# Kernel optimization log

Measured on AMD Instinct MI355X. Metric: run time of the kernel, lower is better.

## Reference

```python
import jax, jax.numpy as jnp
import numpy as np

RADIUS = 0.2
NSAMPLE = 32
GROUPS = 4
EPS = 1e-5


def group_norm(x, gamma, beta):
    # x: [B, C, *spatial]; normalize per (batch, group) over channels-in-group + spatial
    B, C = x.shape[0], x.shape[1]
    rest = x.shape[2:]
    xr = x.reshape(B, GROUPS, -1)
    mean = xr.mean(-1, keepdims=True)
    var = xr.var(-1, keepdims=True)
    xr = (xr - mean) * jax.lax.rsqrt(var + EPS)
    x = xr.reshape((B, C) + rest)
    bshape = (1, C) + (1,) * len(rest)
    return x * gamma.reshape(bshape) + beta.reshape(bshape)


def ball_query(pos_t):
    # pos_t: [B, N, 3] -> idx [B, N, NSAMPLE] (query points == all points)
    N = pos_t.shape[1]
    sq = jnp.sum(pos_t * pos_t, axis=-1)  # [B, N]
    d = sq[:, :, None] + sq[:, None, :] - 2.0 * jnp.einsum('bnc,bmc->bnm', pos_t, pos_t)
    ar = jnp.arange(N, dtype=jnp.int32)
    gi = jnp.where(d > RADIUS * RADIUS, N, ar[None, None, :])  # [B, S, N]
    gi = jnp.sort(gi, axis=-1)[:, :, :NSAMPLE]  # ascending in-ball indices first
    first = gi[:, :, :1]
    gi = jnp.where(gi == N, first, gi)  # pad with first neighbor
    return gi


def setup_inputs() -> dict:
    key = jax.random.key(0)
    ks = jax.random.split(key, 6)
    B, C, N = 2, 64, 4096
    M = 4 * C  # mid channels
    return {
        'x': jax.random.normal(ks[0], (B, C, N), jnp.float32),
        'pos': jax.random.uniform(ks[1], (B, 3, N), jnp.float32),
        'w1': jax.random.normal(ks[2], (M, C), jnp.float32) * 0.05,
        'b1': jnp.zeros((M,), jnp.float32),
        'g1': jnp.ones((M,), jnp.float32),
        'be1': jnp.zeros((M,), jnp.float32),
        'wd': 1.0 + jax.random.normal(ks[3], (M,), jnp.float32) * 0.05,
        'gd': jnp.ones((M,), jnp.float32),
        'bed': jnp.zeros((M,), jnp.float32),
        'w2': jax.random.normal(ks[4], (C, M), jnp.float32) * 0.05,
        'b2': jnp.zeros((C,), jnp.float32),
        'g2': jnp.ones((C,), jnp.float32),
        'be2': jnp.zeros((C,), jnp.float32),
    }


def reference(x, pos, w1, b1, g1, be1, wd, gd, bed, w2, b2, g2, be2):
    # x: [B, C, N], pos: [B, 3, N]
    pos_t = jnp.transpose(pos, (0, 2, 1))  # [B, N, 3]
    idx = ball_query(pos_t)  # [B, N, K]

    # conv1 (1x1) -> GroupNorm -> GELU
    h = jnp.einsum('mc,bcn->bmn', w1, x) + b1[None, :, None]
    h = jax.nn.gelu(group_norm(h, g1, be1), approximate=False)  # [B, M, N]

    # gather neighbors: feats [B, N, M] indexed by idx [B, N, K]
    feats = jnp.transpose(h, (0, 2, 1))
    grouped = jax.vmap(lambda f, i: f[i])(feats, idx)  # [B, N, K, M]
    grouped = jnp.transpose(grouped, (0, 3, 1, 2))  # [B, M, N, K]

    # depthwise 1x1 conv (per-channel scale, no bias) -> GroupNorm -> max-pool over K -> GELU
    grouped = grouped * wd[None, :, None, None]
    grouped = group_norm(grouped, gd, bed)
    h2 = jax.nn.gelu(jnp.max(grouped, axis=-1), approximate=False)  # [B, M, N]

    # conv2 (1x1) -> GroupNorm -> residual
    out = jnp.einsum('cm,bmn->bcn', w2, h2) + b2[None, :, None]
    out = group_norm(out, g2, be2)
    return out + x
```

## Files before the change

kernel.cpp:

```cpp
#include <hip/hip_runtime.h>
#include <hip/hip_fp16.h>
#include <math.h>

#define BB 2
#define CC 64
#define NN 4096
#define MM 256
#define KK 32
#define GG 4
#define EPSF 1e-5f

__device__ __forceinline__ float gelu_exact(float x) {
    return 0.5f * x * (1.0f + erff(x * 0.70710678118654752f));
}

__device__ __forceinline__ unsigned pkmax(unsigned a, unsigned b) {
    unsigned d;
    asm("v_pk_max_f16 %0, %1, %2" : "=v"(d) : "v"(a), "v"(b));
    return d;
}
__device__ __forceinline__ unsigned pkmin(unsigned a, unsigned b) {
    unsigned d;
    asm("v_pk_min_f16 %0, %1, %2" : "=v"(d) : "v"(a), "v"(b));
    return d;
}
__device__ __forceinline__ unsigned selpair(unsigned mx, unsigned mn, float g0, float g1) {
    unsigned lo = (g0 >= 0.f) ? (mx & 0x0000FFFFu) : (mn & 0x0000FFFFu);
    unsigned hi = (g1 >= 0.f) ? (mx & 0xFFFF0000u) : (mn & 0xFFFF0000u);
    return lo | hi;
}
__device__ __forceinline__ float bcast_lane(float v, int lane) {
    return __int_as_float(__builtin_amdgcn_readlane(__float_as_int(v), lane));
}

__global__ void k_mlp1(const float* __restrict__ x, const float* __restrict__ w1,
                       const float* __restrict__ b1, __half* __restrict__ hH,
                       float2* __restrict__ Mp) {
    __shared__ float xs[64 * 128];
    __shared__ float w1t[64 * 32];
    __shared__ float r1[4], r2[4];

    int bx = blockIdx.x;
    int nt = bx & 31, mt = (bx >> 5) & 7, b = bx >> 8;
    int n0 = nt * 128, m0 = mt * 32;
    int t = threadIdx.x;

    {
        int nq = t & 31, ch = t >> 5;
        #pragma unroll
        for (int p = 0; p < 8; p++) {
            int c = p * 8 + ch;
            float4 v = *(const float4*)&x[((size_t)(b * CC + c)) * NN + n0 + nq * 4];
            *(float4*)&xs[c * 128 + nq * 4] = v;
        }
    }
    {
        #pragma unroll
        for (int p = 0; p < 2; p++) {
            int idx = p * 256 + t;
            int m = idx >> 4, cq = idx & 15;
            float4 v = *(const float4*)&w1[(m0 + m) * CC + cq * 4];
            w1t[(cq * 4 + 0) * 32 + m] = v.x;
            w1t[(cq * 4 + 1) * 32 + m] = v.y;
            w1t[(cq * 4 + 2) * 32 + m] = v.z;
            w1t[(cq * 4 + 3) * 32 + m] = v.w;
        }
    }
    __syncthreads();

    int nq = t & 31;
    int mseg = t >> 5;
    float o[4][4];
    #pragma unroll
    for (int i = 0; i < 4; i++)
        #pragma unroll
        for (int j = 0; j < 4; j++) o[i][j] = 0.f;

    for (int c = 0; c < 64; c++) {
        float4 xv = *(float4*)&xs[c * 128 + nq * 4];
        float4 wv = *(float4*)&w1t[c * 32 + mseg * 4];
        o[0][0] = fmaf(wv.x, xv.x, o[0][0]); o[0][1] = fmaf(wv.x, xv.y, o[0][1]);
        o[0][2] = fmaf(wv.x, xv.z, o[0][2]); o[0][3] = fmaf(wv.x, xv.w, o[0][3]);
        o[1][0] = fmaf(wv.y, xv.x, o[1][0]); o[1][1] = fmaf(wv.y, xv.y, o[1][1]);
        o[1][2] = fmaf(wv.y, xv.z, o[1][2]); o[1][3] = fmaf(wv.y, xv.w, o[1][3]);
        o[2][0] = fmaf(wv.z, xv.x, o[2][0]); o[2][1] = fmaf(wv.z, xv.y, o[2][1]);
        o[2][2] = fmaf(wv.z, xv.z, o[2][2]); o[2][3] = fmaf(wv.z, xv.w, o[2][3]);
        o[3][0] = fmaf(wv.w, xv.x, o[3][0]); o[3][1] = fmaf(wv.w, xv.y, o[3][1]);
        o[3][2] = fmaf(wv.w, xv.z, o[3][2]); o[3][3] = fmaf(wv.w, xv.w, o[3][3]);
    }

    float s1 = 0.f, s2 = 0.f;
    #pragma unroll
    for (int mi = 0; mi < 4; mi++) {
        int m = m0 + mseg * 4 + mi;
        float bv = b1[m];
        float4 r;
        r.x = o[mi][0] + bv; r.y = o[mi][1] + bv;
        r.z = o[mi][2] + bv; r.w = o[mi][3] + bv;
        __half2 hA = __float22half2_rn(make_float2(r.x, r.y));
        __half2 hB = __float22half2_rn(make_float2(r.z, r.w));
        uint2 st8;
        st8.x = *(unsigned*)&hA; st8.y = *(unsigned*)&hB;
        *(uint2*)((char*)hH + (((size_t)(b * MM + m)) * NN + n0 + nq * 4) * 2) = st8;
        s1 += r.x + r.y + r.z + r.w;
        s2 = fmaf(r.x, r.x, s2); s2 = fmaf(r.y, r.y, s2);
        s2 = fmaf(r.z, r.z, s2); s2 = fmaf(r.w, r.w, s2);
    }
    for (int off = 32; off; off >>= 1) {
        s1 += __shfl_down(s1, off, 64);
        s2 += __shfl_down(s2, off, 64);
    }
    int w = t >> 6, l = t & 63;
    if (l == 0) { r1[w] = s1; r2[w] = s2; }
    __syncthreads();
    if (t == 0) {
        Mp[bx] = make_float2(r1[0] + r1[1] + r1[2] + r1[3],
                             r2[0] + r2[1] + r2[2] + r2[3]);
    }
}

__global__ void k_gn1t_ballq(const __half* __restrict__ hH, const float* __restrict__ g1,
                             const float* __restrict__ be1, const float* __restrict__ wd,
                             const float2* __restrict__ Mp, __half* __restrict__ pH,
                             float* __restrict__ R,
                             const float* __restrict__ pos, int* __restrict__ idx) {
    __shared__ float tile[64 * 65];
    __shared__ float mv[2];
    int t = threadIdx.x;

    if (blockIdx.x < 512) {
        int id = blockIdx.x;
        int n0 = (id & 63) * 64;
        int g  = (id >> 6) & 3;
        int b  = id >> 8;
        int m0 = g * 64;

        if (t < 64) {
            float2 p2 = Mp[b * 256 + g * 64 + t];
            float s1 = p2.x, s2 = p2.y;
            for (int off = 32; off; off >>= 1) {
                s1 += __shfl_down(s1, off, 64);
                s2 += __shfl_down(s2, off, 64);
            }
            if (t == 0) {
                const double cnt = 64.0 * 4096.0;
                double md = (double)s1 / cnt;
                double vd = (double)s2 / cnt - md * md;
                mv[0] = (float)md;
                mv[1] = rsqrtf((float)vd + EPSF);
            }
        }
        __syncthreads();
        float mean = mv[0], rstd = mv[1];

        int nq = t & 15, mr = t >> 4;
        #pragma unroll
        for (int pp = 0; pp < 4; pp++) {
            int row = pp * 16 + mr;
            int m = m0 + row;
            float a = rstd * g1[m];
            float cc2 = be1[m] - mean * a;
            float wdm = wd[m];
            uint2 raw = *(const uint2*)((const char*)hH +
                         (((size_t)(b * MM + m)) * NN + n0 + nq * 4) * 2);
            float2 fa = __half22float2(*(__half2*)&raw.x);
            float2 fb = __half22float2(*(__half2*)&raw.y);
            tile[row * 65 + nq * 4 + 0] = gelu_exact(fmaf(fa.x, a, cc2)) * wdm;
            tile[row * 65 + nq * 4 + 1] = gelu_exact(fmaf(fa.y, a, cc2)) * wdm;
            tile[row * 65 + nq * 4 + 2] = gelu_exact(fmaf(fb.x, a, cc2)) * wdm;
            tile[row * 65 + nq * 4 + 3] = gelu_exact(fmaf(fb.y, a, cc2)) * wdm;
        }
        __syncthreads();
        #pragma unroll
        for (int pp = 0; pp < 4; pp++) {
            int id2 = pp * 256 + t;
            int nl = id2 >> 4, mq = id2 & 15;
            float a0 = tile[(mq * 4 + 0) * 65 + nl];
            float a1 = tile[(mq * 4 + 1) * 65 + nl];
            float a2 = tile[(mq * 4 + 2) * 65 + nl];
            float a3 = tile[(mq * 4 + 3) * 65 + nl];
            __half2 hA = __float22half2_rn(make_float2(a0, a1));
            __half2 hB = __float22half2_rn(make_float2(a2, a3));
            uint2 st8;
            st8.x = *(unsigned*)&hA; st8.y = *(unsigned*)&hB;
            *(uint2*)((char*)pH + ((((size_t)(b * NN) + n0 + nl)) << 9) + (m0 + mq * 4) * 2) = st8;
            float2 fa = __half22float2(hA);
            float2 fb = __half22float2(hB);
            float t1 = fa.x + fa.y + fb.x + fb.y;
            float t2 = fa.x * fa.x + fa.y * fa.y + fb.x * fb.x + fb.y * fb.y;
            #pragma unroll
            for (int off = 8; off; off >>= 1) {
                t1 += __shfl_down(t1, off, 16);
                t2 += __shfl_down(t2, off, 16);
            }
            if ((t & 15) == 0) {
                float* rr = &R[((size_t)(b * NN) + n0 + nl) * 8];
                rr[g]     = t1;
                rr[4 + g] = t2;
            }
        }
    } else {
        int bx = blockIdx.x - 512;
        int wid  = bx * 4 + (threadIdx.x >> 6);
        int lane = threadIdx.x & 63;
        int b = wid >> 12;
        int n = wid & 4095;
        const float* px = pos + b * 3 * NN;
        const float* py = px + NN;
        const float* pz = py + NN;
        float qx = px[n], qy = py[n], qz = pz[n];
        float qsq = qx*qx + qy*qy + qz*qz;
        int* row = idx + (b * NN + n) * KK;

        int found = 0;
        int first = -1;
        const float R2 = 0.04f;
        for (int m0 = 0; m0 < NN && found < KK; m0 += 64) {
            int m = m0 + lane;
            float ax = px[m], ay = py[m], az = pz[m];
            float msq = ax*ax + ay*ay + az*az;
            float dot = qx*ax + qy*ay + qz*az;
            float d = qsq + msq - 2.0f * dot;
            bool hit = !(d > R2);
            unsigned long long mask = __ballot(hit);
            if (first < 0 && mask) first = m0 + (__ffsll((long long)mask) - 1);
            unsigned long long lt = (lane == 0) ? 0ULL : (mask & ((1ULL << lane) - 1ULL));
            int posh = __popcll(lt);
            if (hit && (found + posh) < KK) row[found + posh] = m;
            found += __popcll(mask);
            if (found > KK) found = KK;
        }
        if (lane < KK && lane >= found) row[lane] = first;
    }
}

__global__ void k_gstats(const int* __restrict__ idx, const float* __restrict__ R,
                         float* __restrict__ Gp) {
    __shared__ float sAcc[8][8];
    int t = threadIdx.x;
    int bid = blockIdx.x;
    int hw = t >> 5, cl = t & 31;
    int pbase = bid * 32;
    int b = pbase >> 12;
    float s[8];
    #pragma unroll
    for (int c = 0; c < 8; c++) s[c] = 0.f;
    #pragma unroll
    for (int it = 0; it < 4; it++) {
        int pt = pbase + it * 8 + hw;
        int j = idx[pt * KK + cl];
        const float* rr = &R[((size_t)(b * NN) + j) * 8];
        float4 ra = *(const float4*)rr;
        float4 rb = *(const float4*)(rr + 4);
        s[0] += ra.x; s[1] += ra.y; s[2] += ra.z; s[3] += ra.w;
        s[4] += rb.x; s[5] += rb.y; s[6] += rb.z; s[7] += rb.w;
    }
    #pragma unroll
    for (int off = 16; off; off >>= 1) {
        #pragma unroll
        for (int c = 0; c < 8; c++) s[c] += __shfl_down(s[c], off, 32);
    }
    if (cl == 0) {
        #pragma unroll
        for (int c = 0; c < 8; c++) sAcc[hw][c] = s[c];
    }
    __syncthreads();
    if (t < 8) {
        float v = 0.f;
        #pragma unroll
        for (int k = 0; k < 8; k++) v += sAcc[k][t];
        Gp[bid * 8 + t] = v;
    }
}

__global__ __launch_bounds__(256, 2)
void k_mlp2g(const __half* __restrict__ pH, const int* __restrict__ idx,
             const float* __restrict__ Gp, const float* __restrict__ w2,
             const float* __restrict__ b2, const float* __restrict__ gd,
             const float* __restrict__ bed, float* __restrict__ oraw,
             float* __restrict__ Op) {
    __shared__ float w2s[64 * 257];
    __shared__ uint4 phs4[4][4][32];
    __shared__ float sw[4][8];
    __shared__ float sA[4][4], sB[4][4];

    int t = threadIdx.x;
    int w = t >> 6, l = t & 63;
    int q = blockIdx.x;
    int b = ((q & 7) < 4) ? 0 : 1;
    int local = (q >> 3) * 4 + (q & 3);
    int n0 = local * 16 + w * 4;

    #pragma unroll
    for (int p = 0; p < 16; p++) {
        int i = p * 256 + t;
        int c = i >> 6, mq = i & 63;
        float4 v = ((const float4*)w2)[i];
        float* dst = &w2s[c * 257 + mq * 4];
        dst[0] = v.x; dst[1] = v.y; dst[2] = v.z; dst[3] = v.w;
    }

    {
        float s[8] = {0.f, 0.f, 0.f, 0.f, 0.f, 0.f, 0.f, 0.f};
        if (t < 128) {
            const float4* gp = (const float4*)(Gp + ((size_t)(b * 128 + t)) * 8);
            float4 ra = gp[0], rb = gp[1];
            s[0] = ra.x; s[1] = ra.y; s[2] = ra.z; s[3] = ra.w;
            s[4] = rb.x; s[5] = rb.y; s[6] = rb.z; s[7] = rb.w;
        }
        #pragma unroll
        for (int off = 32; off; off >>= 1) {
            #pragma unroll
            for (int c = 0; c < 8; c++) s[c] += __shfl_down(s[c], off, 64);
        }
        if (l == 0) {
            #pragma unroll
            for (int c = 0; c < 8; c++) sw[w][c] = s[c];
        }
    }
    __syncthreads();

    int g = l >> 4;
    double s1 = (double)sw[0][g] + sw[1][g] + sw[2][g] + sw[3][g];
    double s2 = (double)sw[0][4 + g] + sw[1][4 + g] + sw[2][4 + g] + sw[3][4 + g];
    const double cnt2 = 64.0 * 4096.0 * 32.0;
    double m_ = s1 / cnt2;
    double v_ = s2 / cnt2 - m_ * m_;
    float mean = (float)m_;
    float rstd = rsqrtf((float)v_ + EPSF);
    float4 gd4  = ((const float4*)gd)[l];
    float4 bed4 = ((const float4*)bed)[l];
    float ax = rstd * gd4.x, ay = rstd * gd4.y, az = rstd * gd4.z, aw = rstd * gd4.w;
    float cx = bed4.x - mean * ax, cy = bed4.y - mean * ay;
    float cz = bed4.z - mean * az, cw = bed4.w - mean * aw;

    {
        int hh = l >> 5, cl = l & 31;
        const char* pb = (const char*)(pH + (size_t)b * NN * 256);
        int laneoff = cl * 16;
        const float4* g4 = (const float4*)gd;
        float4 gA = g4[cl * 2], gB = g4[cl * 2 + 1];
        #pragma unroll
        for (int p = 0; p < 4; p++) {
            int myidx = idx[((size_t)(b * NN) + n0 + p) * KK + cl];
            unsigned vmax0 = 0xFC00FC00u, vmax1 = 0xFC00FC00u, vmax2 = 0xFC00FC00u, vmax3 = 0xFC00FC00u;
            unsigned vmin0 = 0x7C007C00u, vmin1 = 0x7C007C00u, vmin2 = 0x7C007C00u, vmin3 = 0x7C007C00u;
            #pragma unroll
            for (int kb = 0; kb < 4; kb++) {
                int jj[4];
                #pragma unroll
                for (int u = 0; u < 4; u++) {
                    int k = kb * 4 + u;
                    int ja = __shfl(myidx, 2 * k, 64);
                    int jb = __shfl(myidx, 2 * k + 1, 64);
                    jj[u] = hh ? jb : ja;
                }
                uint4 r[4];
                #pragma unroll
                for (int u = 0; u < 4; u++)
                    r[u] = *(const uint4*)(pb + (((size_t)jj[u]) << 9) + laneoff);
                #pragma unroll
                for (int u = 0; u < 4; u++) {
                    vmax0 = pkmax(vmax0, r[u].x); vmin0 = pkmin(vmin0, r[u].x);
                    vmax1 = pkmax(vmax1, r[u].y); vmin1 = pkmin(vmin1, r[u].y);
                    vmax2 = pkmax(vmax2, r[u].z); vmin2 = pkmin(vmin2, r[u].z);
                    vmax3 = pkmax(vmax3, r[u].w); vmin3 = pkmin(vmin3, r[u].w);
                }
            }
            vmax0 = pkmax(vmax0, (unsigned)__shfl_xor((int)vmax0, 32, 64));
            vmax1 = pkmax(vmax1, (unsigned)__shfl_xor((int)vmax1, 32, 64));
            vmax2 = pkmax(vmax2, (unsigned)__shfl_xor((int)vmax2, 32, 64));
            vmax3 = pkmax(vmax3, (unsigned)__shfl_xor((int)vmax3, 32, 64));
            vmin0 = pkmin(vmin0, (unsigned)__shfl_xor((int)vmin0, 32, 64));
            vmin1 = pkmin(vmin1, (unsigned)__shfl_xor((int)vmin1, 32, 64));
            vmin2 = pkmin(vmin2, (unsigned)__shfl_xor((int)vmin2, 32, 64));
            vmin3 = pkmin(vmin3, (unsigned)__shfl_xor((int)vmin3, 32, 64));

            if (hh == 0) {
                uint4 o4;
                o4.x = selpair(vmax0, vmin0, gA.x, gA.y);
                o4.y = selpair(vmax1, vmin1, gA.z, gA.w);
                o4.z = selpair(vmax2, vmin2, gB.x, gB.y);
                o4.w = selpair(vmax3, vmin3, gB.z, gB.w);
                phs4[w][p][cl] = o4;
            }
        }
    }

    float4 h2r[4];
    #pragma unroll
    for (int j = 0; j < 4; j++) {
        const uint2* pr = (const uint2*)&phs4[w][j][0];
        uint2 raw = pr[l];
        float2 fa = __half22float2(*(__half2*)&raw.x);
        float2 fb = __half22float2(*(__half2*)&raw.y);
        h2r[j].x = gelu_exact(fmaf(fa.x, ax, cx));
        h2r[j].y = gelu_exact(fmaf(fa.y, ay, cy));
        h2r[j].z = gelu_exact(fmaf(fb.x, az, cz));
        h2r[j].w = gelu_exact(fmaf(fb.y, aw, cw));
    }

    const float* w2l = &w2s[l * 257];
    float acc[4] = {0.f, 0.f, 0.f, 0.f};
    #pragma unroll 8
    for (int mq = 0; mq < 64; mq++) {
        float w0  = w2l[4 * mq + 0];
        float w1_ = w2l[4 * mq + 1];
        float w2_ = w2l[4 * mq + 2];
        float w3_ = w2l[4 * mq + 3];
        #pragma unroll
        for (int j = 0; j < 4; j++) {
            acc[j] = fmaf(w0,  bcast_lane(h2r[j].x, mq), acc[j]);
            acc[j] = fmaf(w1_, bcast_lane(h2r[j].y, mq), acc[j]);
            acc[j] = fmaf(w2_, bcast_lane(h2r[j].z, mq), acc[j]);
            acc[j] = fmaf(w3_, bcast_lane(h2r[j].w, mq), acc[j]);
        }
    }

    float bias = b2[l];
    float so1 = 0.f, so2 = 0.f;
    #pragma unroll
    for (int j = 0; j < 4; j++) {
        acc[j] += bias;
        so1 += acc[j];
        so2 = fmaf(acc[j], acc[j], so2);
    }
    *(float4*)&oraw[((size_t)(b * CC) + l) * NN + n0] =
        make_float4(acc[0], acc[1], acc[2], acc[3]);

    so1 += __shfl_down(so1, 8, 16); so2 += __shfl_down(so2, 8, 16);
    so1 += __shfl_down(so1, 4, 16); so2 += __shfl_down(so2, 4, 16);
    so1 += __shfl_down(so1, 2, 16); so2 += __shfl_down(so2, 2, 16);
    so1 += __shfl_down(so1, 1, 16); so2 += __shfl_down(so2, 1, 16);
    if ((l & 15) == 0) { sA[w][l >> 4] = so1; sB[w][l >> 4] = so2; }
    __syncthreads();
    if (t < 8) {
        int is2 = t >> 2, gg = t & 3;
        float v = is2 ? (sB[0][gg] + sB[1][gg] + sB[2][gg] + sB[3][gg])
                      : (sA[0][gg] + sA[1][gg] + sA[2][gg] + sA[3][gg]);
        Op[(b * 256 + local) * 8 + t] = v;
    }
}

__global__ void k_final(const float* __restrict__ oraw, const float* __restrict__ x,
                        const float* __restrict__ g2, const float* __restrict__ be2,
                        const float* __restrict__ Op, float* __restrict__ out) {
    __shared__ float fw[4][8];
    int t = threadIdx.x;
    int i4 = blockIdx.x * 256 + t;
    int base = i4 * 4;
    int b = base >> 18;

    {
        const float4* rp = (const float4*)(Op + ((size_t)(b * 256 + t)) * 8);
        float4 ra = rp[0], rb = rp[1];
        float s[8] = {ra.x, ra.y, ra.z, ra.w, rb.x, rb.y, rb.z, rb.w};
        #pragma unroll
        for (int off = 32; off; off >>= 1) {
            #pragma unroll
            for (int c = 0; c < 8; c++) s[c] += __shfl_down(s[c], off, 64);
        }
        if ((t & 63) == 0) {
            #pragma unroll
            for (int c = 0; c < 8; c++) fw[t >> 6][c] = s[c];
        }
    }
    __syncthreads();

    int c = (base >> 12) & 63;
    int g = c >> 4;
    double s1 = (double)fw[0][g] + fw[1][g] + fw[2][g] + fw[3][g];
    double s2 = (double)fw[0][4 + g] + fw[1][4 + g] + fw[2][4 + g] + fw[3][4 + g];
    const double cnt = 16.0 * 4096.0;
    double mean_d = s1 / cnt;
    double var_d  = s2 / cnt - mean_d * mean_d;
    float mean = (float)mean_d;
    float rstd = rsqrtf((float)var_d + EPSF);
    float sc = rstd * g2[c];
    float ad = be2[c] - mean * sc;
    float4 o = ((const float4*)oraw)[i4];
    float4 xv = ((const float4*)x)[i4];
    float4 r;
    r.x = fmaf(o.x, sc, ad) + xv.x;
    r.y = fmaf(o.y, sc, ad) + xv.y;
    r.z = fmaf(o.z, sc, ad) + xv.z;
    r.w = fmaf(o.w, sc, ad) + xv.w;
    ((float4*)out)[i4] = r;
}

extern "C" void kernel_launch(void* const* d_in, const int* in_sizes, int n_in,
                              void* d_out, int out_size, void* d_ws, size_t ws_size,
                              hipStream_t stream) {
    const float* x   = (const float*)d_in[0];
    const float* pos = (const float*)d_in[1];
    const float* w1  = (const float*)d_in[2];
    const float* b1  = (const float*)d_in[3];
    const float* g1  = (const float*)d_in[4];
    const float* be1 = (const float*)d_in[5];
    const float* wd  = (const float*)d_in[6];
    const float* gd  = (const float*)d_in[7];
    const float* bed = (const float*)d_in[8];
    const float* w2  = (const float*)d_in[9];
    const float* b2  = (const float*)d_in[10];
    const float* g2  = (const float*)d_in[11];
    const float* be2 = (const float*)d_in[12];
    float* out = (float*)d_out;

    char* wsb = (char*)d_ws;
    __half* hH    = (__half*)wsb;
    __half* pH    = (__half*)(wsb + 8388608);
    float*  oraw  = (float*)(wsb + 16777216);
    int*    idx   = (int*)(wsb + 18874368);
    float*  R     = (float*)(wsb + 19922944);
    float2* Mp    = (float2*)(wsb + 20185088);
    float*  Gp    = (float*)(wsb + 20189184);
    float*  Op    = (float*)(wsb + 20197376);

    k_mlp1<<<512, 256, 0, stream>>>(x, w1, b1, hH, Mp);
    k_gn1t_ballq<<<2560, 256, 0, stream>>>(hH, g1, be1, wd, Mp, pH, R, pos, idx);
    k_gstats<<<256, 256, 0, stream>>>(idx, R, Gp);
    k_mlp2g<<<512, 256, 0, stream>>>(pH, idx, Gp, w2, b2, gd, bed, oraw, Op);
    k_final<<<512, 256, 0, stream>>>(oraw, x, g2, be2, Op, out);
}
```

Measured before the change: 146.1 us.

## Fuse ball query into conv1 kernel and compute grouped stats via neighbor counts

Ball query now runs in the same launch as the conv1 GEMM, and each neighbor hit atomically bumps a per-point occurrence count. The GN1/transpose kernel then weights each point's channel-group sums by that count to get the grouped GroupNorm statistics directly. This removes the separate gather-based stats kernel and the per-point R buffer. Conv2 and final stats are now accumulated with global atomics into a small buffer instead of partial arrays reduced again downstream. The cost is many global atomics, a memset launch, and float atomic ordering making the statistics slightly nondeterministic.

Result: slower. 214.5 us (+46.8%).

```diff
diff --git a/kernel.cpp b/kernel.cpp
--- a/kernel.cpp
+++ b/kernel.cpp
@@ -33,171 +33,94 @@
     return __int_as_float(__builtin_amdgcn_readlane(__float_as_int(v), lane));
 }
 
-__global__ void k_mlp1(const float* __restrict__ x, const float* __restrict__ w1,
-                       const float* __restrict__ b1, __half* __restrict__ hH,
-                       float2* __restrict__ Mp) {
-    __shared__ float xs[64 * 128];
-    __shared__ float w1t[64 * 32];
-    __shared__ float r1[4], r2[4];
-
-    int bx = blockIdx.x;
-    int nt = bx & 31, mt = (bx >> 5) & 7, b = bx >> 8;
-    int n0 = nt * 128, m0 = mt * 32;
+__global__ void k_mlp1_ballq(const float* __restrict__ x, const float* __restrict__ w1,
+                             const float* __restrict__ b1, __half* __restrict__ hH,
+                             float2* __restrict__ Mp,
+                             const float* __restrict__ pos, int* __restrict__ idxb,
+                             int* __restrict__ cnt) {
+    __shared__ __align__(16) float xs[64 * 128];
+    __shared__ __align__(16) float w1t[64 * 32];
     int t = threadIdx.x;
 
-    {
-        int nq = t & 31, ch = t >> 5;
+    if (blockIdx.x < 512) {
+        int bx = blockIdx.x;
+        int nt = bx & 31, mt = (bx >> 5) & 7, b = bx >> 8;
+        int n0 = nt * 128, m0 = mt * 32;
+
+        {
+            int nq = t & 31, ch = t >> 5;
+            #pragma unroll
+            for (int p = 0; p < 8; p++) {
+                int c = p * 8 + ch;
+                float4 v = *(const float4*)&x[((size_t)(b * CC + c)) * NN + n0 + nq * 4];
+                *(float4*)&xs[c * 128 + nq * 4] = v;
+            }
+        }
+        {
+            #pragma unroll
+            for (int p = 0; p < 2; p++) {
+                int idx = p * 256 + t;
+                int m = idx >> 4, cq = idx & 15;
+                float4 v = *(const float4*)&w1[(m0 + m) * CC + cq * 4];
+                w1t[(cq * 4 + 0) * 32 + m] = v.x;
+                w1t[(cq * 4 + 1) * 32 + m] = v.y;
+                w1t[(cq * 4 + 2) * 32 + m] = v.z;
+                w1t[(cq * 4 + 3) * 32 + m] = v.w;
+            }
+        }
+        __syncthreads();
+
+        int nq = t & 31;
+        int mseg = t >> 5;
+        float o[4][4];
         #pragma unroll
-        for (int p = 0; p < 8; p++) {
-            int c = p * 8 + ch;
-            float4 v = *(const float4*)&x[((size_t)(b * CC + c)) * NN + n0 + nq * 4];
-            *(float4*)&xs[c * 128 + nq * 4] = v;
-        }
-    }
-    {
+        for (int i = 0; i < 4; i++)
+            #pragma unroll
+            for (int j = 0; j < 4; j++) o[i][j] = 0.f;
+
+        for (int c = 0; c < 64; c++) {
+            float4 xv = *(float4*)&xs[c * 128 + nq * 4];
+            float4 wv = *(float4*)&w1t[c * 32 + mseg * 4];
+            o[0][0] = fmaf(wv.x, xv.x, o[0][0]); o[0][1] = fmaf(wv.x, xv.y, o[0][1]);
+            o[0][2] = fmaf(wv.x, xv.z, o[0][2]); o[0][3] = fmaf(wv.x, xv.w, o[0][3]);
+            o[1][0] = fmaf(wv.y, xv.x, o[1][0]); o[1][1] = fmaf(wv.y, xv.y, o[1][1]);
+            o[1][2] = fmaf(wv.y, xv.z, o[1][2]); o[1][3] = fmaf(wv.y, xv.w, o[1][3]);
+            o[2][0] = fmaf(wv.z, xv.x, o[2][0]); o[2][1] = fmaf(wv.z, xv.y, o[2][1]);
+            o[2][2] = fmaf(wv.z, xv.z, o[2][2]); o[2][3] = fmaf(wv.z, xv.w, o[2][3]);
+            o[3][0] = fmaf(wv.w, xv.x, o[3][0]); o[3][1] = fmaf(wv.w, xv.y, o[3][1]);
+            o[3][2] = fmaf(wv.w, xv.z, o[3][2]); o[3][3] = fmaf(wv.w, xv.w, o[3][3]);
+        }
+
+        float s1 = 0.f, s2 = 0.f;
         #pragma unroll
-        for (int p = 0; p < 2; p++) {
-            int idx = p * 256 + t;
-            int m = idx >> 4, cq = idx & 15;
-            float4 v = *(const float4*)&w1[(m0 + m) * CC + cq * 4];
-            w1t[(cq * 4 + 0) * 32 + m] = v.x;
-            w1t[(cq * 4 + 1) * 32 + m] = v.y;
-            w1t[(cq * 4 + 2) * 32 + m] = v.z;
-            w1t[(cq * 4 + 3) * 32 + m] = v.w;
-        }
-    }
-    __syncthreads();
-
-    int nq = t & 31;
-    int mseg = t >> 5;
-    float o[4][4];
-    #pragma unroll
-    for (int i = 0; i < 4; i++)
-        #pragma unroll
-        for (int j = 0; j < 4; j++) o[i][j] = 0.f;
-
-    for (int c = 0; c < 64; c++) {
-        float4 xv = *(float4*)&xs[c * 128 + nq * 4];
-        float4 wv = *(float4*)&w1t[c * 32 + mseg * 4];
-        o[0][0] = fmaf(wv.x, xv.x, o[0][0]); o[0][1] = fmaf(wv.x, xv.y, o[0][1]);
-        o[0][2] = fmaf(wv.x, xv.z, o[0][2]); o[0][3] = fmaf(wv.x, xv.w, o[0][3]);
-        o[1][0] = fmaf(wv.y, xv.x, o[1][0]); o[1][1] = fmaf(wv.y, xv.y, o[1][1]);
-        o[1][2] = fmaf(wv.y, xv.z, o[1][2]); o[1][3] = fmaf(wv.y, xv.w, o[1][3]);
-        o[2][0] = fmaf(wv.z, xv.x, o[2][0]); o[2][1] = fmaf(wv.z, xv.y, o[2][1]);
-        o[2][2] = fmaf(wv.z, xv.z, o[2][2]); o[2][3] = fmaf(wv.z, xv.w, o[2][3]);
-        o[3][0] = fmaf(wv.w, xv.x, o[3][0]); o[3][1] = fmaf(wv.w, xv.y, o[3][1]);
-        o[3][2] = fmaf(wv.w, xv.z, o[3][2]); o[3][3] = fmaf(wv.w, xv.w, o[3][3]);
-    }
-
-    float s1 = 0.f, s2 = 0.f;
-    #pragma unroll
-    for (int mi = 0; mi < 4; mi++) {
-        int m = m0 + mseg * 4 + mi;
-        float bv = b1[m];
-        float4 r;
-        r.x = o[mi][0] + bv; r.y = o[mi][1] + bv;
-        r.z = o[mi][2] + bv; r.w = o[mi][3] + bv;
-        __half2 hA = __float22half2_rn(make_float2(r.x, r.y));
-        __half2 hB = __float22half2_rn(make_float2(r.z, r.w));
-        uint2 st8;
-        st8.x = *(unsigned*)&hA; st8.y = *(unsigned*)&hB;
-        *(uint2*)((char*)hH + (((size_t)(b * MM + m)) * NN + n0 + nq * 4) * 2) = st8;
-        s1 += r.x + r.y + r.z + r.w;
-        s2 = fmaf(r.x, r.x, s2); s2 = fmaf(r.y, r.y, s2);
-        s2 = fmaf(r.z, r.z, s2); s2 = fmaf(r.w, r.w, s2);
-    }
-    for (int off = 32; off; off >>= 1) {
-        s1 += __shfl_down(s1, off, 64);
-        s2 += __shfl_down(s2, off, 64);
-    }
-    int w = t >> 6, l = t & 63;
-    if (l == 0) { r1[w] = s1; r2[w] = s2; }
-    __syncthreads();
-    if (t == 0) {
-        Mp[bx] = make_float2(r1[0] + r1[1] + r1[2] + r1[3],
-                             r2[0] + r2[1] + r2[2] + r2[3]);
-    }
-}
-
-__global__ void k_gn1t_ballq(const __half* __restrict__ hH, const float* __restrict__ g1,
-                             const float* __restrict__ be1, const float* __restrict__ wd,
-                             const float2* __restrict__ Mp, __half* __restrict__ pH,
-                             float* __restrict__ R,
-                             const float* __restrict__ pos, int* __restrict__ idx) {
-    __shared__ float tile[64 * 65];
-    __shared__ float mv[2];
-    int t = threadIdx.x;
-
-    if (blockIdx.x < 512) {
-        int id = blockIdx.x;
-        int n0 = (id & 63) * 64;
-        int g  = (id >> 6) & 3;
-        int b  = id >> 8;
-        int m0 = g * 64;
-
-        if (t < 64) {
-            float2 p2 = Mp[b * 256 + g * 64 + t];
-            float s1 = p2.x, s2 = p2.y;
-            for (int off = 32; off; off >>= 1) {
-                s1 += __shfl_down(s1, off, 64);
-                s2 += __shfl_down(s2, off, 64);
-            }
-            if (t == 0) {
-                const double cnt = 64.0 * 4096.0;
-                double md = (double)s1 / cnt;
-                double vd = (double)s2 / cnt - md * md;
-                mv[0] = (float)md;
-                mv[1] = rsqrtf((float)vd + EPSF);
-            }
-        }
-        __syncthreads();
-        float mean = mv[0], rstd = mv[1];
-
-        int nq = t & 15, mr = t >> 4;
-        #pragma unroll
-        for (int pp = 0; pp < 4; pp++) {
-            int row = pp * 16 + mr;
-            int m = m0 + row;
-            float a = rstd * g1[m];
-            float cc2 = be1[m] - mean * a;
-            float wdm = wd[m];
-            uint2 raw = *(const uint2*)((const char*)hH +
-                         (((size_t)(b * MM + m)) * NN + n0 + nq * 4) * 2);
-            float2 fa = __half22float2(*(__half2*)&raw.x);
-            float2 fb = __half22float2(*(__half2*)&raw.y);
-            tile[row * 65 + nq * 4 + 0] = gelu_exact(fmaf(fa.x, a, cc2)) * wdm;
-            tile[row * 65 + nq * 4 + 1] = gelu_exact(fmaf(fa.y, a, cc2)) * wdm;
-            tile[row * 65 + nq * 4 + 2] = gelu_exact(fmaf(fb.x, a, cc2)) * wdm;
-            tile[row * 65 + nq * 4 + 3] = gelu_exact(fmaf(fb.y, a, cc2)) * wdm;
-        }
-        __syncthreads();
-        #pragma unroll
-        for (int pp = 0; pp < 4; pp++) {
-            int id2 = pp * 256 + t;
-            int nl = id2 >> 4, mq = id2 & 15;
-            float a0 = tile[(mq * 4 + 0) * 65 + nl];
-            float a1 = tile[(mq * 4 + 1) * 65 + nl];
-            float a2 = tile[(mq * 4 + 2) * 65 + nl];
-            float a3 = tile[(mq * 4 + 3) * 65 + nl];
-            __half2 hA = __float22half2_rn(make_float2(a0, a1));
-            __half2 hB = __float22half2_rn(make_float2(a2, a3));
+        for (int mi = 0; mi < 4; mi++) {
+            int m = m0 + mseg * 4 + mi;
+            float bv = b1[m];
+            float4 r;
+            r.x = o[mi][0] + bv; r.y = o[mi][1] + bv;
+            r.z = o[mi][2] + bv; r.w = o[mi][3] + bv;
+            __half2 hA = __float22half2_rn(make_float2(r.x, r.y));
+            __half2 hB = __float22half2_rn(make_float2(r.z, r.w));
             uint2 st8;
             st8.x = *(unsigned*)&hA; st8.y = *(unsigned*)&hB;
-            *(uint2*)((char*)pH + ((((size_t)(b * NN) + n0 + nl)) << 9) + (m0 + mq * 4) * 2) = st8;
-            float2 fa = __half22float2(hA);
-            float2 fb = __half22float2(hB);
-            float t1 = fa.x + fa.y + fb.x + fb.y;
-            float t2 = fa.x * fa.x + fa.y * fa.y + fb.x * fb.x + fb.y * fb.y;
-            #pragma unroll
-            for (int off = 8; off; off >>= 1) {
-                t1 += __shfl_down(t1, off, 16);
-                t2 += __shfl_down(t2, off, 16);
-            }
-            if ((t & 15) == 0) {
-                float* rr = &R[((size_t)(b * NN) + n0 + nl) * 8];
-                rr[g]     = t1;
-                rr[4 + g] = t2;
-            }
+            *(uint2*)((char*)hH + (((size_t)(b * MM + m)) * NN + n0 + nq * 4) * 2) = st8;
+            s1 += r.x + r.y + r.z + r.w;
+            s2 = fmaf(r.x, r.x, s2); s2 = fmaf(r.y, r.y, s2);
+            s2 = fmaf(r.z, r.z, s2); s2 = fmaf(r.w, r.w, s2);
+        }
+        for (int off = 32; off; off >>= 1) {
+            s1 += __shfl_down(s1, off, 64);
+            s2 += __shfl_down(s2, off, 64);
+        }
+        __syncthreads();
+        float* r1 = w1t;
+        float* r2 = w1t + 4;
+        int w = t >> 6, l = t & 63;
+        if (l == 0) { r1[w] = s1; r2[w] = s2; }
+        __syncthreads();
+        if (t == 0) {
+            Mp[bx] = make_float2(r1[0] + r1[1] + r1[2] + r1[3],
+                                 r2[0] + r2[1] + r2[2] + r2[3]);
         }
     } else {
         int bx = blockIdx.x - 512;
@@ -210,7 +133,8 @@
         const float* pz = py + NN;
         float qx = px[n], qy = py[n], qz = pz[n];
         float qsq = qx*qx + qy*qy + qz*qz;
-        int* row = idx + (b * NN + n) * KK;
+        int* row = idxb + (b * NN + n) * KK;
+        int* cb = cnt + b * NN;
 
         int found = 0;
         int first = -1;
@@ -226,62 +150,113 @@
             if (first < 0 && mask) first = m0 + (__ffsll((long long)mask) - 1);
             unsigned long long lt = (lane == 0) ? 0ULL : (mask & ((1ULL << lane) - 1ULL));
             int posh = __popcll(lt);
-            if (hit && (found + posh) < KK) row[found + posh] = m;
+            if (hit && (found + posh) < KK) {
+                row[found + posh] = m;
+                atomicAdd(&cb[m], 1);
+            }
             found += __popcll(mask);
             if (found > KK) found = KK;
         }
         if (lane < KK && lane >= found) row[lane] = first;
-    }
-}
-
-__global__ void k_gstats(const int* __restrict__ idx, const float* __restrict__ R,
-                         float* __restrict__ Gp) {
-    __shared__ float sAcc[8][8];
+        if (lane == 0 && found < KK) atomicAdd(&cb[first], KK - found);
+    }
+}
+
+__global__ void k_gn1t(const __half* __restrict__ hH, const float* __restrict__ g1,
+                       const float* __restrict__ be1, const float* __restrict__ wd,
+                       const float2* __restrict__ Mp, __half* __restrict__ pH,
+                       const int* __restrict__ cnt, float* __restrict__ GpS) {
+    __shared__ float tile[64 * 65];
+    __shared__ float mv[2];
+    __shared__ float sAcc1, sAcc2;
     int t = threadIdx.x;
-    int bid = blockIdx.x;
-    int hw = t >> 5, cl = t & 31;
-    int pbase = bid * 32;
-    int b = pbase >> 12;
-    float s[8];
+
+    int id = blockIdx.x;
+    int n0 = (id & 63) * 64;
+    int g  = (id >> 6) & 3;
+    int b  = id >> 8;
+    int m0 = g * 64;
+
+    if (t == 0) { sAcc1 = 0.f; sAcc2 = 0.f; }
+    if (t < 64) {
+        float2 p2 = Mp[b * 256 + g * 64 + t];
+        float s1 = p2.x, s2 = p2.y;
+        for (int off = 32; off; off >>= 1) {
+            s1 += __shfl_down(s1, off, 64);
+            s2 += __shfl_down(s2, off, 64);
+        }
+        if (t == 0) {
+            const double cntd = 64.0 * 4096.0;
+            double md = (double)s1 / cntd;
+            double vd = (double)s2 / cntd - md * md;
+            mv[0] = (float)md;
+            mv[1] = rsqrtf((float)vd + EPSF);
+        }
+    }
+    __syncthreads();
+    float mean = mv[0], rstd = mv[1];
+
+    int nq = t & 15, mr = t >> 4;
     #pragma unroll
-    for (int c = 0; c < 8; c++) s[c] = 0.f;
+    for (int pp = 0; pp < 4; pp++) {
+        int row = pp * 16 + mr;
+        int m = m0 + row;
+        float a = rstd * g1[m];
+        float cc2 = be1[m] - mean * a;
+        float wdm = wd[m];
+        uint2 raw = *(const uint2*)((const char*)hH +
+                     (((size_t)(b * MM + m)) * NN + n0 + nq * 4) * 2);
+        float2 fa = __half22float2(*(__half2*)&raw.x);
+        float2 fb = __half22float2(*(__half2*)&raw.y);
+        tile[row * 65 + nq * 4 + 0] = gelu_exact(fmaf(fa.x, a, cc2)) * wdm;
+        tile[row * 65 + nq * 4 + 1] = gelu_exact(fmaf(fa.y, a, cc2)) * wdm;
+        tile[row * 65 + nq * 4 + 2] = gelu_exact(fmaf(fb.x, a, cc2)) * wdm;
+        tile[row * 65 + nq * 4 + 3] = gelu_exact(fmaf(fb.y, a, cc2)) * wdm;
+    }
+    __syncthreads();
     #pragma unroll
-    for (int it = 0; it < 4; it++) {
-        int pt = pbase + it * 8 + hw;
-        int j = idx[pt * KK + cl];
-        const float* rr = &R[((size_t)(b * NN) + j) * 8];
-        float4 ra = *(const float4*)rr;
-        float4 rb = *(const float4*)(rr + 4);
-        s[0] += ra.x; s[1] += ra.y; s[2] += ra.z; s[3] += ra.w;
-        s[4] += rb.x; s[5] += rb.y; s[6] += rb.z; s[7] += rb.w;
-    }
-    #pragma unroll
-    for (int off = 16; off; off >>= 1) {
+    for (int pp = 0; pp < 4; pp++) {
+        int id2 = pp * 256 + t;
+        int nl = id2 >> 4, mq = id2 & 15;
+        float a0 = tile[(mq * 4 + 0) * 65 + nl];
+        float a1 = tile[(mq * 4 + 1) * 65 + nl];
+        float a2 = tile[(mq * 4 + 2) * 65 + nl];
+        float a3 = tile[(mq * 4 + 3) * 65 + nl];
+        __half2 hA = __float22half2_rn(make_float2(a0, a1));
+        __half2 hB = __float22half2_rn(make_float2(a2, a3));
+        uint2 st8;
+        st8.x = *(unsigned*)&hA; st8.y = *(unsigned*)&hB;
+        *(uint2*)((char*)pH + ((((size_t)(b * NN) + n0 + nl)) << 9) + (m0 + mq * 4) * 2) = st8;
+        float2 fa = __half22float2(hA);
+        float2 fb = __half22float2(hB);
+        float t1 = fa.x + fa.y + fb.x + fb.y;
+        float t2 = fa.x * fa.x + fa.y * fa.y + fb.x * fb.x + fb.y * fb.y;
         #pragma unroll
-        for (int c = 0; c < 8; c++) s[c] += __shfl_down(s[c], off, 32);
-    }
-    if (cl == 0) {
-        #pragma unroll
-        for (int c = 0; c < 8; c++) sAcc[hw][c] = s[c];
+        for (int off = 8; off; off >>= 1) {
+            t1 += __shfl_down(t1, off, 16);
+            t2 += __shfl_down(t2, off, 16);
+        }
+        if ((t & 15) == 0) {
+            float cw = (float)cnt[b * NN + n0 + nl];
+            atomicAdd(&sAcc1, cw * t1);
+            atomicAdd(&sAcc2, cw * t2);
+        }
     }
     __syncthreads();
-    if (t < 8) {
-        float v = 0.f;
-        #pragma unroll
-        for (int k = 0; k < 8; k++) v += sAcc[k][t];
-        Gp[bid * 8 + t] = v;
+    if (t == 0) {
+        atomicAdd(&GpS[b * 8 + g],     sAcc1);
+        atomicAdd(&GpS[b * 8 + 4 + g], sAcc2);
     }
 }
 
 __global__ __launch_bounds__(256, 2)
-void k_mlp2g(const __half* __restrict__ pH, const int* __restrict__ idx,
-             const float* __restrict__ Gp, const float* __restrict__ w2,
+void k_mlp2g(const __half* __restrict__ pH, const int* __restrict__ idxb,
+             const float* __restrict__ GpS, const float* __restrict__ w2,
              const float* __restrict__ b2, const float* __restrict__ gd,
              const float* __restrict__ bed, float* __restrict__ oraw,
-             float* __restrict__ Op) {
+             float* __restrict__ OpS) {
     __shared__ float w2s[64 * 257];
     __shared__ uint4 phs4[4][4][32];
-    __shared__ float sw[4][8];
     __shared__ float sA[4][4], sB[4][4];
 
     int t = threadIdx.x;
@@ -299,30 +274,11 @@
         float* dst = &w2s[c * 257 + mq * 4];
         dst[0] = v.x; dst[1] = v.y; dst[2] = v.z; dst[3] = v.w;
     }
-
-    {
-        float s[8] = {0.f, 0.f, 0.f, 0.f, 0.f, 0.f, 0.f, 0.f};
-        if (t < 128) {
-            const float4* gp = (const float4*)(Gp + ((size_t)(b * 128 + t)) * 8);
-            float4 ra = gp[0], rb = gp[1];
-            s[0] = ra.x; s[1] = ra.y; s[2] = ra.z; s[3] = ra.w;
-            s[4] = rb.x; s[5] = rb.y; s[6] = rb.z; s[7] = rb.w;
-        }
-        #pragma unroll
-        for (int off = 32; off; off >>= 1) {
-            #pragma unroll
-            for (int c = 0; c < 8; c++) s[c] += __shfl_down(s[c], off, 64);
-        }
-        if (l == 0) {
-            #pragma unroll
-            for (int c = 0; c < 8; c++) sw[w][c] = s[c];
-        }
-    }
     __syncthreads();
 
     int g = l >> 4;
-    double s1 = (double)sw[0][g] + sw[1][g] + sw[2][g] + sw[3][g];
-    double s2 = (double)sw[0][4 + g] + sw[1][4 + g] + sw[2][4 + g] + sw[3][4 + g];
+    double s1 = (double)GpS[b * 8 + g];
+    double s2 = (double)GpS[b * 8 + 4 + g];
     const double cnt2 = 64.0 * 4096.0 * 32.0;
     double m_ = s1 / cnt2;
     double v_ = s2 / cnt2 - m_ * m_;
@@ -342,7 +298,7 @@
         float4 gA = g4[cl * 2], gB = g4[cl * 2 + 1];
         #pragma unroll
         for (int p = 0; p < 4; p++) {
-            int myidx = idx[((size_t)(b * NN) + n0 + p) * KK + cl];
+            int myidx = idxb[((size_t)(b * NN) + n0 + p) * KK + cl];
             unsigned vmax0 = 0xFC00FC00u, vmax1 = 0xFC00FC00u, vmax2 = 0xFC00FC00u, vmax3 = 0xFC00FC00u;
             unsigned vmin0 = 0x7C007C00u, vmin1 = 0x7C007C00u, vmin2 = 0x7C007C00u, vmin3 = 0x7C007C00u;
             #pragma unroll
@@ -438,42 +394,25 @@
         int is2 = t >> 2, gg = t & 3;
         float v = is2 ? (sB[0][gg] + sB[1][gg] + sB[2][gg] + sB[3][gg])
                       : (sA[0][gg] + sA[1][gg] + sA[2][gg] + sA[3][gg]);
-        Op[(b * 256 + local) * 8 + t] = v;
+        atomicAdd(&OpS[b * 8 + t], v);
     }
 }
 
 __global__ void k_final(const float* __restrict__ oraw, const float* __restrict__ x,
                         const float* __restrict__ g2, const float* __restrict__ be2,
-                        const float* __restrict__ Op, float* __restrict__ out) {
-    __shared__ float fw[4][8];
+                        const float* __restrict__ OpS, float* __restrict__ out) {
     int t = threadIdx.x;
     int i4 = blockIdx.x * 256 + t;
     int base = i4 * 4;
     int b = base >> 18;
-
-    {
-        const float4* rp = (const float4*)(Op + ((size_t)(b * 256 + t)) * 8);
-        float4 ra = rp[0], rb = rp[1];
-        float s[8] = {ra.x, ra.y, ra.z, ra.w, rb.x, rb.y, rb.z, rb.w};
-        #pragma unroll
-        for (int off = 32; off; off >>= 1) {
-            #pragma unroll
-            for (int c = 0; c < 8; c++) s[c] += __shfl_down(s[c], off, 64);
-        }
-        if ((t & 63) == 0) {
-            #pragma unroll
-            for (int c = 0; c < 8; c++) fw[t >> 6][c] = s[c];
-        }
-    }
-    __syncthreads();
-
     int c = (base >> 12) & 63;
     int g = c >> 4;
-    double s1 = (double)fw[0][g] + fw[1][g] + fw[2][g] + fw[3][g];
-    double s2 = (double)fw[0][4 + g] + fw[1][4 + g] + fw[2][4 + g] + fw[3][4 + g];
-    const double cnt = 16.0 * 4096.0;
-    double mean_d = s1 / cnt;
-    double var_d  = s2 / cnt - mean_d * mean_d;
+
+    double s1 = (double)OpS[b * 8 + g];
+    double s2 = (double)OpS[b * 8 + 4 + g];
+    const double cntd = 16.0 * 4096.0;
+    double mean_d = s1 / cntd;
+    double var_d  = s2 / cntd - mean_d * mean_d;
     float mean = (float)mean_d;
     float rstd = rsqrtf((float)var_d + EPSF);
     float sc = rstd * g2[c];
@@ -510,15 +449,16 @@
     __half* hH    = (__half*)wsb;
     __half* pH    = (__half*)(wsb + 8388608);
     float*  oraw  = (float*)(wsb + 16777216);
-    int*    idx   = (int*)(wsb + 18874368);
-    float*  R     = (float*)(wsb + 19922944);
+    int*    idxb  = (int*)(wsb + 18874368);
     float2* Mp    = (float2*)(wsb + 20185088);
-    float*  Gp    = (float*)(wsb + 20189184);
-    float*  Op    = (float*)(wsb + 20197376);
-
-    k_mlp1<<<512, 256, 0, stream>>>(x, w1, b1, hH, Mp);
-    k_gn1t_ballq<<<2560, 256, 0, stream>>>(hH, g1, be1, wd, Mp, pH, R, pos, idx);
-    k_gstats<<<256, 256, 0, stream>>>(idx, R, Gp);
-    k_mlp2g<<<512, 256, 0, stream>>>(pH, idx, Gp, w2, b2, gd, bed, oraw, Op);
-    k_final<<<512, 256, 0, stream>>>(oraw, x, g2, be2, Op, out);
-}
+    int*    cnt   = (int*)(wsb + 20189184);
+    float*  GpS   = (float*)(wsb + 20221952);
+    float*  OpS   = (float*)(wsb + 20222016);
+
+    hipMemsetAsync((void*)cnt, 0, 32896, stream);
+
+    k_mlp1_ballq<<<2560, 256, 0, stream>>>(x, w1, b1, hH, Mp, pos, idxb, cnt);
+    k_gn1t<<<512, 256, 0, stream>>>(hH, g1, be1, wd, Mp, pH, cnt, GpS);
+    k_mlp2g<<<512, 256, 0, stream>>>(pH, idxb, GpS, w2, b2, gd, bed, oraw, OpS);
+    k_final<<<512, 256, 0, stream>>>(oraw, x, g2, be2, OpS, out);
+}
```
